# Optimization experiments

Hardware: AMD Instinct MI355X
Metric: run time of the kernel (lower is better)

Reference implementation:

```python
import jax, jax.numpy as jnp
import numpy as np

N_NODES = 50000
N_EDGES = 800000
FEAT = 128
HID = 128
N_GRAPHS = 512
N_CLASSES = 10
N_BLOCKS = 3
N_INNER = 2
BN_EPS = 1e-5


def setup_inputs() -> dict:
    key = jax.random.key(0)
    ks = jax.random.split(key, 16)
    return {
        "x": jax.random.normal(ks[0], (N_NODES, FEAT), dtype=jnp.float32),
        "edge_attr": jax.random.uniform(ks[1], (N_EDGES,), dtype=jnp.float32),
        "conv_w": jax.random.normal(ks[2], (N_BLOCKS, N_INNER, HID, HID), dtype=jnp.float32) * 0.05,
        "conv_b": jax.random.normal(ks[3], (N_BLOCKS, N_INNER, HID), dtype=jnp.float32) * 0.05,
        "jk_w": jax.random.normal(ks[4], (N_BLOCKS, N_INNER * HID, HID), dtype=jnp.float32) * 0.05,
        "jk_b": jax.random.normal(ks[5], (N_BLOCKS, HID), dtype=jnp.float32) * 0.05,
        "bn_gamma": jnp.ones((N_BLOCKS * HID,), dtype=jnp.float32),
        "bn_beta": jnp.zeros((N_BLOCKS * HID,), dtype=jnp.float32),
        "bn_mean": jnp.zeros((N_BLOCKS * HID,), dtype=jnp.float32),
        "bn_var": jnp.ones((N_BLOCKS * HID,), dtype=jnp.float32),
        "lin1_w": jax.random.normal(ks[6], (N_BLOCKS * HID, HID), dtype=jnp.float32) * 0.05,
        "lin1_b": jnp.zeros((HID,), dtype=jnp.float32),
        "lin2_w": jax.random.normal(ks[7], (HID, N_CLASSES), dtype=jnp.float32) * 0.05,
        "lin2_b": jnp.zeros((N_CLASSES,), dtype=jnp.float32),
        "edge_index": jax.random.randint(ks[8], (2, N_EDGES), 0, N_NODES, dtype=jnp.int32),
        "batch": jnp.sort(jax.random.randint(ks[9], (N_NODES,), 0, N_GRAPHS, dtype=jnp.int32)),
    }


def _gcn_conv(x, w, b, src, dst, ew):
    """GCNConv with edge weights and self-loops: D^-1/2 (A+I) D^-1/2 X W + b."""
    n = x.shape[0]
    xw = x @ w  # [N, H]
    deg = jax.ops.segment_sum(ew, dst, num_segments=n) + 1.0  # self-loop weight 1
    dinv = jax.lax.rsqrt(deg)  # [N]
    norm = dinv[src] * ew * dinv[dst]  # [E]
    agg = jax.ops.segment_sum(xw[src] * norm[:, None], dst, num_segments=n)
    agg = agg + xw * (dinv * dinv)[:, None]  # self-loop term
    return agg + b


def reference(x, edge_attr, conv_w, conv_b, jk_w, jk_b, bn_gamma, bn_beta,
              bn_mean, bn_var, lin1_w, lin1_b, lin2_w, lin2_b,
              edge_index, batch):
    src, dst = edge_index[0], edge_index[1]
    h = x
    pooled = []
    for l in range(N_BLOCKS):
        xs = []
        for k in range(N_INNER):
            h = jax.nn.relu(_gcn_conv(h, conv_w[l, k], conv_b[l, k], src, dst, edge_attr))
            xs.append(h)
        # JumpingKnowledge 'cat' + Linear + ReLU
        h = jax.nn.relu(jnp.concatenate(xs, axis=-1) @ jk_w[l] + jk_b[l])
        # global add pool per graph
        pooled.append(jax.ops.segment_sum(h, batch, num_segments=N_GRAPHS))
    z = jnp.concatenate(pooled, axis=1)  # [B, 3*HID]
    # BatchNorm1d (eval mode)
    z = (z - bn_mean) * jax.lax.rsqrt(bn_var + BN_EPS) * bn_gamma + bn_beta
    z = jax.nn.relu(z @ lin1_w + lin1_b)
    z = z @ lin2_w + lin2_b
    return jax.nn.softmax(z, axis=-1)
```

## Files before the change

kernel.cpp:

```cpp
#include <hip/hip_runtime.h>
#include <hip/hip_fp16.h>

static constexpr int NN = 50000;
static constexpr int NE = 800000;
static constexpr int NG = 512;

typedef unsigned int uint;
typedef unsigned short ushort;
typedef unsigned long long u64;
typedef __attribute__((ext_vector_type(8))) short short8;
typedef __attribute__((ext_vector_type(4))) float f32x4;

__device__ inline uint bfbits(float f) {
    uint u = __float_as_uint(f);
    return (u + 0x7fffu + ((u >> 16) & 1u)) >> 16;
}
__device__ inline float bflo(uint g) { return __uint_as_float(g << 16); }
__device__ inline float bfhi(uint g) { return __uint_as_float(g & 0xffff0000u); }
__device__ inline float bf2f(ushort s) { return __uint_as_float(((uint)s) << 16); }

__global__ void hist_kernel(const int* __restrict__ dst, const float* __restrict__ ew,
                            u64* __restrict__ pk, ushort* __restrict__ rankb, int nE)
{
    int i = blockIdx.x * blockDim.x + threadIdx.x;
    if (i < nE) {
        int d = dst[i];
        u64 v = (1ULL << 40) + (u64)(ew[i] * 16777216.0f + 0.5f);
        u64 old = atomicAdd(&pk[d], v);
        rankb[i] = (ushort)(old >> 40);
    }
}

__global__ __launch_bounds__(256) void scan_bsum_kernel(const u64* __restrict__ pk,
                                                        int* __restrict__ bsum,
                                                        float* __restrict__ dinv, int n)
{
    __shared__ int wred[4];
    int i = blockIdx.x * 256 + threadIdx.x;
    int v = 0;
    if (i < n) {
        u64 p = pk[i];
        v = (int)(p >> 40);
        float deg = (float)(p & 0xFFFFFFFFFFULL) * (1.0f / 16777216.0f) + 1.0f;
        dinv[i] = rsqrtf(deg);
    }
    int s = v;
    #pragma unroll
    for (int o = 32; o > 0; o >>= 1) s += __shfl_down(s, o, 64);
    int wid = threadIdx.x >> 6;
    if ((threadIdx.x & 63) == 0) wred[wid] = s;
    __syncthreads();
    if (threadIdx.x == 0)
        bsum[blockIdx.x] = wred[0] + wred[1] + wred[2] + wred[3];
}

__global__ __launch_bounds__(256) void scan_boff_kernel(const int* __restrict__ bsum,
                                                        int* __restrict__ boff, int nbs)
{
    __shared__ int sh[256];
    int tid = threadIdx.x;
    int v = (tid < nbs) ? bsum[tid] : 0;
    sh[tid] = v;
    __syncthreads();
    #pragma unroll
    for (int o = 1; o < 256; o <<= 1) {
        int t = (tid >= o) ? sh[tid - o] : 0;
        __syncthreads();
        sh[tid] += t;
        __syncthreads();
    }
    if (tid < nbs) boff[tid] = sh[tid] - v;
    if (tid == 255) boff[nbs] = sh[255];
}

__global__ __launch_bounds__(256) void scan_final_kernel(const u64* __restrict__ pk,
                                                         const int* __restrict__ boff,
                                                         int* __restrict__ rowptr,
                                                         int n, int nbs)
{
    __shared__ int sh[256];
    int tid = threadIdx.x;
    int i = blockIdx.x * 256 + tid;
    int v = (i < n) ? (int)(pk[i] >> 40) : 0;
    sh[tid] = v;
    __syncthreads();
    #pragma unroll
    for (int o = 1; o < 256; o <<= 1) {
        int t = (tid >= o) ? sh[tid - o] : 0;
        __syncthreads();
        sh[tid] += t;
        __syncthreads();
    }
    if (i < n) rowptr[i] = boff[blockIdx.x] + sh[tid] - v;
    if (blockIdx.x == 0 && tid == 0) rowptr[n] = boff[nbs];
}

__global__ void fill_kernel(const int* __restrict__ src, const int* __restrict__ dst,
                            const float* __restrict__ ew, const float* __restrict__ dinv,
                            const int* __restrict__ rowptr,
                            const ushort* __restrict__ rankb,
                            uint* __restrict__ ecv, int nE)
{
    int i = blockIdx.x * blockDim.x + threadIdx.x;
    if (i < nE) {
        int s = src[i], d = dst[i];
        int pos = rowptr[d] + (int)rankb[i];
        float v = ew[i] * dinv[s];
        ecv[pos] = (uint)s | ((uint)__half_as_ushort(__float2half_rn(v)) << 16);
    }
}

__global__ void cvtx_kernel(const float* __restrict__ x, ushort* __restrict__ xb, int n)
{
    int i = (blockIdx.x * blockDim.x + threadIdx.x) * 4;
    if (i < n) {
        float4 v = *(const float4*)&x[i];
        uint2 p;
        p.x = bfbits(v.x) | (bfbits(v.y) << 16);
        p.y = bfbits(v.z) | (bfbits(v.w) << 16);
        *(uint2*)&xb[i] = p;
    }
}

__global__ void wfrag_kernel(const float* __restrict__ src, ushort* __restrict__ dst,
                             int K, int wstride_src, int wstride_dst)
{
    int wid = blockIdx.y;
    const float* s = src + (size_t)wid * wstride_src;
    ushort* d = dst + (size_t)wid * wstride_dst;
    int i = blockIdx.x * 256 + threadIdx.x;
    int e = i & 7;
    int lane = (i >> 3) & 63;
    int rest = i >> 9;
    int nt = K >> 5;
    int t = rest % nt;
    int j = rest / nt;
    int k = t * 32 + (lane >> 4) * 8 + e;
    int col = j * 16 + (lane & 15);
    d[i] = (ushort)bfbits(s[(size_t)k * 128 + col]);
}

template<bool RELU, bool BIAS>
__global__ __launch_bounds__(256) void gemm_mfma_kernel(
    const ushort* __restrict__ Ab, int K, int lda,
    const ushort* __restrict__ Wb, const float* __restrict__ bias,
    ushort* __restrict__ outb, int nrows)
{
    const int wid  = threadIdx.x >> 6;
    const int lane = threadIdx.x & 63;
    const int row0 = blockIdx.x * 64 + wid * 16;
    const int c    = lane & 15;
    const int kg   = lane >> 4;
    int arow = row0 + c;
    if (arow >= nrows) arow = nrows - 1;
    const ushort* Aptr = Ab + (size_t)arow * lda + kg * 8;
    const int nt = K >> 5;

    f32x4 acc[8];
    #pragma unroll
    for (int j = 0; j < 8; ++j) acc[j] = (f32x4)0.f;

    for (int t = 0; t < nt; ++t) {
        short8 a = *(const short8*)(Aptr + t * 32);
        const ushort* Wp = Wb + ((size_t)t * 64 + lane) * 8;
        #pragma unroll
        for (int j = 0; j < 8; ++j) {
            short8 b = *(const short8*)(Wp + (size_t)j * nt * 512);
            acc[j] = __builtin_amdgcn_mfma_f32_16x16x32_bf16(a, b, acc[j], 0, 0, 0);
        }
    }
    #pragma unroll
    for (int r = 0; r < 4; ++r) {
        int orow = row0 + kg * 4 + r;
        if (orow >= nrows) continue;
        #pragma unroll
        for (int j = 0; j < 8; ++j) {
            float v = acc[j][r];
            int col = j * 16 + c;
            if (BIAS) v += bias[col];
            if (RELU) v = fmaxf(v, 0.f);
            outb[(size_t)orow * 128 + col] = (ushort)bfbits(v);
        }
    }
}

__global__ __launch_bounds__(256) void agg_kernel(
    const uint* __restrict__ xwb, const int* __restrict__ rowptr,
    const uint* __restrict__ ecv,
    const float* __restrict__ dinv, const float* __restrict__ bias,
    uint* __restrict__ outu, int ldo, int coff, int n)
{
    int node = (int)((blockIdx.x * (size_t)blockDim.x + threadIdx.x) >> 6);
    int lane = threadIdx.x & 63;
    if (node >= n) return;
    float d = dinv[node];
    uint  g = xwb[(size_t)node * 64 + lane];
    float bx = 0.f, by = 0.f;
    int e0 = rowptr[node], e1 = rowptr[node + 1];
    int e = e0;
    for (; e + 8 <= e1; e += 8) {
        uint rec[8];
        #pragma unroll
        for (int q = 0; q < 8; ++q) rec[q] = ecv[e + q];
        uint gq[8];
        #pragma unroll
        for (int q = 0; q < 8; ++q)
            gq[q] = xwb[(size_t)(rec[q] & 0xffffu) * 64 + lane];
        #pragma unroll
        for (int q = 0; q < 8; ++q) {
            float v = __half2float(__ushort_as_half((ushort)(rec[q] >> 16)));
            bx = fmaf(v, bflo(gq[q]), bx);
            by = fmaf(v, bfhi(gq[q]), by);
        }
    }
    for (; e + 4 <= e1; e += 4) {
        uint rec[4];
        #pragma unroll
        for (int q = 0; q < 4; ++q) rec[q] = ecv[e + q];
        uint gq[4];
        #pragma unroll
        for (int q = 0; q < 4; ++q)
            gq[q] = xwb[(size_t)(rec[q] & 0xffffu) * 64 + lane];
        #pragma unroll
        for (int q = 0; q < 4; ++q) {
            float v = __half2float(__ushort_as_half((ushort)(rec[q] >> 16)));
            bx = fmaf(v, bflo(gq[q]), bx);
            by = fmaf(v, bfhi(gq[q]), by);
        }
    }
    for (; e < e1; ++e) {
        uint rec = ecv[e];
        uint gg = xwb[(size_t)(rec & 0xffffu) * 64 + lane];
        float v = __half2float(__ushort_as_half((ushort)(rec >> 16)));
        bx = fmaf(v, bflo(gg), bx);
        by = fmaf(v, bfhi(gg), by);
    }
    float sw = d * d;
    float ax = fmaf(d, bx, bflo(g) * sw);
    float ay = fmaf(d, by, bfhi(g) * sw);
    float2 b = *(const float2*)&bias[lane * 2];
    ax = fmaxf(ax + b.x, 0.f);
    ay = fmaxf(ay + b.y, 0.f);
    outu[(size_t)node * ldo + coff + lane] = bfbits(ax) | (bfbits(ay) << 16);
}

static constexpr int NPP = 32;
__global__ __launch_bounds__(128) void pool_kernel(
    const ushort* __restrict__ h, const int* __restrict__ batch,
    float* __restrict__ z, int zoff, int n)
{
    int f  = threadIdx.x;
    int n0 = blockIdx.x * NPP;
    if (n0 >= n) return;
    int nend = n0 + NPP; if (nend > n) nend = n;
    int cur = batch[n0];
    float acc = 0.f;
    for (int node = n0; node < nend; ++node) {
        int b = batch[node];
        if (b != cur) {
            atomicAdd(&z[(size_t)cur * 384 + zoff + f], acc);
            acc = 0.f; cur = b;
        }
        acc += bf2f(h[(size_t)node * 128 + f]);
    }
    atomicAdd(&z[(size_t)cur * 384 + zoff + f], acc);
}

__global__ __launch_bounds__(128) void head_kernel(
    const float* __restrict__ z,
    const float* __restrict__ g,  const float* __restrict__ be,
    const float* __restrict__ mu, const float* __restrict__ var,
    const float* __restrict__ w1, const float* __restrict__ b1,
    const float* __restrict__ w2, const float* __restrict__ b2,
    float* __restrict__ out)
{
    int gi = blockIdx.x;
    int t  = threadIdx.x;
    __shared__ float zs[384];
    __shared__ float h1[128];
    __shared__ float lg[10];
    for (int i = t; i < 384; i += 128) {
        float v = z[(size_t)gi * 384 + i];
        v = (v - mu[i]) * rsqrtf(var[i] + 1e-5f) * g[i] + be[i];
        zs[i] = v;
    }
    __syncthreads();
    float acc = b1[t];
    for (int k = 0; k < 384; ++k) acc = fmaf(zs[k], w1[(size_t)k * 128 + t], acc);
    h1[t] = fmaxf(acc, 0.f);
    __syncthreads();
    if (t < 10) {
        float a2 = b2[t];
        for (int k = 0; k < 128; ++k) a2 = fmaf(h1[k], w2[(size_t)k * 10 + t], a2);
        lg[t] = a2;
    }
    __syncthreads();
    if (t == 0) {
        float m = lg[0];
        for (int i = 1; i < 10; ++i) m = fmaxf(m, lg[i]);
        float e[10], s = 0.f;
        for (int i = 0; i < 10; ++i) { e[i] = expf(lg[i] - m); s += e[i]; }
        float inv = 1.f / s;
        for (int i = 0; i < 10; ++i) out[(size_t)gi * 10 + i] = e[i] * inv;
    }
}

extern "C" void kernel_launch(void* const* d_in, const int* in_sizes, int n_in,
                              void* d_out, int out_size, void* d_ws, size_t ws_size,
                              hipStream_t stream)
{
    const float* x      = (const float*)d_in[0];
    const float* ea     = (const float*)d_in[1];
    const float* conv_w = (const float*)d_in[2];
    const float* conv_b = (const float*)d_in[3];
    const float* jk_w   = (const float*)d_in[4];
    const float* jk_b   = (const float*)d_in[5];
    const float* bn_g   = (const float*)d_in[6];
    const float* bn_b   = (const float*)d_in[7];
    const float* bn_m   = (const float*)d_in[8];
    const float* bn_v   = (const float*)d_in[9];
    const float* w1     = (const float*)d_in[10];
    const float* b1     = (const float*)d_in[11];
    const float* w2     = (const float*)d_in[12];
    const float* b2     = (const float*)d_in[13];
    const int*   eidx   = (const int*)d_in[14];
    const int*   batch  = (const int*)d_in[15];
    const int* srcv = eidx;
    const int* dstv = eidx + NE;
    float* out = (float*)d_out;

    char* ws = (char*)d_ws;
    size_t off = 0;
    auto alloc = [&](size_t b) { size_t o = off; off += (b + 511) & ~(size_t)511; return o; };
    u64*   pk     = (u64*)  (ws + alloc((size_t)NN * 8));
    float* z      = (float*)(ws + alloc((size_t)NG * 384 * 4));
    size_t zero_bytes = off;
    float* dinv   = (float*)(ws + alloc((size_t)NN * 4));
    int*   rowptr = (int*)  (ws + alloc((size_t)(NN + 1) * 4));
    ushort* rankb = (ushort*)(ws + alloc((size_t)NE * 2));
    uint*  ecv    = (uint*) (ws + alloc((size_t)NE * 4));
    ushort* xb    = (ushort*)(ws + alloc((size_t)NN * 128 * 2));
    ushort* wbc   = (ushort*)(ws + alloc((size_t)6 * 128 * 128 * 2));
    ushort* wbj   = (ushort*)(ws + alloc((size_t)3 * 256 * 128 * 2));
    uint*  xwb    = (uint*) (ws + alloc((size_t)NN * 64 * 4));
    uint*  xsb    = (uint*) (ws + alloc((size_t)NN * 128 * 4));
    ushort* houtb = (ushort*)(ws + alloc((size_t)NN * 128 * 2));
    int*   bsum   = (int*)  (ws + alloc((size_t)256 * 4));
    int*   boff   = (int*)  (ws + alloc((size_t)257 * 4));
    (void)ws_size; (void)in_sizes; (void)n_in; (void)out_size;

    hipMemsetAsync(d_ws, 0, zero_bytes, stream);

    const int EB  = (NE + 255) / 256;
    const int NB  = (NN + 255) / 256;
    hist_kernel<<<EB, 256, 0, stream>>>(dstv, ea, pk, rankb, NE);
    scan_bsum_kernel<<<NB, 256, 0, stream>>>(pk, bsum, dinv, NN);
    scan_boff_kernel<<<1, 256, 0, stream>>>(bsum, boff, NB);
    scan_final_kernel<<<NB, 256, 0, stream>>>(pk, boff, rowptr, NN, NB);
    fill_kernel<<<EB, 256, 0, stream>>>(srcv, dstv, ea, dinv, rowptr, rankb,
                                        ecv, NE);
    cvtx_kernel<<<(NN * 32 + 255) / 256, 256, 0, stream>>>(x, xb, NN * 128);
    wfrag_kernel<<<dim3(64, 6),  256, 0, stream>>>(conv_w, wbc, 128, 128 * 128, 128 * 128);
    wfrag_kernel<<<dim3(128, 3), 256, 0, stream>>>(jk_w,   wbj, 256, 256 * 128, 256 * 128);

    const int GB = (NN + 63) / 64;
    const int AB = (NN * 64 + 255) / 256;
    const int PB = (NN + NPP - 1) / NPP;

    const ushort* hin = xb;
    int lda = 128;
    for (int l = 0; l < 3; ++l) {
        for (int k = 0; k < 2; ++k) {
            gemm_mfma_kernel<false, false><<<GB, 256, 0, stream>>>(
                hin, 128, lda, wbc + (size_t)(l * 2 + k) * 128 * 128, nullptr,
                (ushort*)xwb, NN);
            agg_kernel<<<AB, 256, 0, stream>>>(
                xwb, rowptr, ecv, dinv, conv_b + (size_t)(l * 2 + k) * 128,
                xsb, 128, k * 64, NN);
            hin = (const ushort*)xsb;
            lda = 256;
        }
        gemm_mfma_kernel<true, true><<<GB, 256, 0, stream>>>(
            (const ushort*)xsb, 256, 256, wbj + (size_t)l * 256 * 128,
            jk_b + (size_t)l * 128, houtb, NN);
        pool_kernel<<<PB, 128, 0, stream>>>(houtb, batch, z, l * 128, NN);
        hin = houtb;
        lda = 128;
    }
    head_kernel<<<NG, 128, 0, stream>>>(z, bn_g, bn_b, bn_m, bn_v,
                                        w1, b1, w2, b2, out);
}
```

Baseline: 588.6 us.

## Fuse JK GEMM with pooling and next conv GEMM; merge prep kernels

```diff
diff --git a/kernel.cpp b/kernel.cpp
--- a/kernel.cpp
+++ b/kernel.cpp
@@ -19,116 +19,43 @@
 __device__ inline float bfhi(uint g) { return __uint_as_float(g & 0xffff0000u); }
 __device__ inline float bf2f(ushort s) { return __uint_as_float(((uint)s) << 16); }
 
-__global__ void hist_kernel(const int* __restrict__ dst, const float* __restrict__ ew,
-                            u64* __restrict__ pk, ushort* __restrict__ rankb, int nE)
-{
-    int i = blockIdx.x * blockDim.x + threadIdx.x;
-    if (i < nE) {
-        int d = dst[i];
-        u64 v = (1ULL << 40) + (u64)(ew[i] * 16777216.0f + 0.5f);
-        u64 old = atomicAdd(&pk[d], v);
-        rankb[i] = (ushort)(old >> 40);
-    }
-}
-
-__global__ __launch_bounds__(256) void scan_bsum_kernel(const u64* __restrict__ pk,
-                                                        int* __restrict__ bsum,
-                                                        float* __restrict__ dinv, int n)
-{
-    __shared__ int wred[4];
-    int i = blockIdx.x * 256 + threadIdx.x;
-    int v = 0;
-    if (i < n) {
-        u64 p = pk[i];
-        v = (int)(p >> 40);
-        float deg = (float)(p & 0xFFFFFFFFFFULL) * (1.0f / 16777216.0f) + 1.0f;
-        dinv[i] = rsqrtf(deg);
-    }
-    int s = v;
-    #pragma unroll
-    for (int o = 32; o > 0; o >>= 1) s += __shfl_down(s, o, 64);
-    int wid = threadIdx.x >> 6;
-    if ((threadIdx.x & 63) == 0) wred[wid] = s;
-    __syncthreads();
-    if (threadIdx.x == 0)
-        bsum[blockIdx.x] = wred[0] + wred[1] + wred[2] + wred[3];
-}
-
-__global__ __launch_bounds__(256) void scan_boff_kernel(const int* __restrict__ bsum,
-                                                        int* __restrict__ boff, int nbs)
-{
-    __shared__ int sh[256];
+static constexpr int EB  = (NE + 255) / 256;
+static constexpr int WBC = 6 * 64;
+static constexpr int WBJ = 3 * 128;
+
+__global__ __launch_bounds__(256) void prep_kernel(
+    const int* __restrict__ dst, const float* __restrict__ ew,
+    u64* __restrict__ pk, ushort* __restrict__ rankb,
+    const float* __restrict__ conv_w, ushort* __restrict__ wbc,
+    const float* __restrict__ jk_w, ushort* __restrict__ wbj)
+{
+    int b = blockIdx.x;
     int tid = threadIdx.x;
-    int v = (tid < nbs) ? bsum[tid] : 0;
-    sh[tid] = v;
-    __syncthreads();
-    #pragma unroll
-    for (int o = 1; o < 256; o <<= 1) {
-        int t = (tid >= o) ? sh[tid - o] : 0;
-        __syncthreads();
-        sh[tid] += t;
-        __syncthreads();
-    }
-    if (tid < nbs) boff[tid] = sh[tid] - v;
-    if (tid == 255) boff[nbs] = sh[255];
-}
-
-__global__ __launch_bounds__(256) void scan_final_kernel(const u64* __restrict__ pk,
-                                                         const int* __restrict__ boff,
-                                                         int* __restrict__ rowptr,
-                                                         int n, int nbs)
-{
-    __shared__ int sh[256];
-    int tid = threadIdx.x;
-    int i = blockIdx.x * 256 + tid;
-    int v = (i < n) ? (int)(pk[i] >> 40) : 0;
-    sh[tid] = v;
-    __syncthreads();
-    #pragma unroll
-    for (int o = 1; o < 256; o <<= 1) {
-        int t = (tid >= o) ? sh[tid - o] : 0;
-        __syncthreads();
-        sh[tid] += t;
-        __syncthreads();
-    }
-    if (i < n) rowptr[i] = boff[blockIdx.x] + sh[tid] - v;
-    if (blockIdx.x == 0 && tid == 0) rowptr[n] = boff[nbs];
-}
-
-__global__ void fill_kernel(const int* __restrict__ src, const int* __restrict__ dst,
-                            const float* __restrict__ ew, const float* __restrict__ dinv,
-                            const int* __restrict__ rowptr,
-                            const ushort* __restrict__ rankb,
-                            uint* __restrict__ ecv, int nE)
-{
-    int i = blockIdx.x * blockDim.x + threadIdx.x;
-    if (i < nE) {
-        int s = src[i], d = dst[i];
-        int pos = rowptr[d] + (int)rankb[i];
-        float v = ew[i] * dinv[s];
-        ecv[pos] = (uint)s | ((uint)__half_as_ushort(__float2half_rn(v)) << 16);
-    }
-}
-
-__global__ void cvtx_kernel(const float* __restrict__ x, ushort* __restrict__ xb, int n)
-{
-    int i = (blockIdx.x * blockDim.x + threadIdx.x) * 4;
-    if (i < n) {
-        float4 v = *(const float4*)&x[i];
-        uint2 p;
-        p.x = bfbits(v.x) | (bfbits(v.y) << 16);
-        p.y = bfbits(v.z) | (bfbits(v.w) << 16);
-        *(uint2*)&xb[i] = p;
-    }
-}
-
-__global__ void wfrag_kernel(const float* __restrict__ src, ushort* __restrict__ dst,
-                             int K, int wstride_src, int wstride_dst)
-{
-    int wid = blockIdx.y;
-    const float* s = src + (size_t)wid * wstride_src;
-    ushort* d = dst + (size_t)wid * wstride_dst;
-    int i = blockIdx.x * 256 + threadIdx.x;
+    if (b < EB) {
+        int i = b * 256 + tid;
+        if (i < NE) {
+            int d = dst[i];
+            u64 v = (1ULL << 40) + (u64)(ew[i] * 16777216.0f + 0.5f);
+            u64 old = atomicAdd(&pk[d], v);
+            rankb[i] = (ushort)(old >> 40);
+        }
+        return;
+    }
+    const float* s; ushort* d; int K, blk;
+    if (b < EB + WBC) {
+        int bb = b - EB;
+        int wid = bb >> 6; blk = bb & 63;
+        K = 128;
+        s = conv_w + (size_t)wid * 128 * 128;
+        d = wbc    + (size_t)wid * 128 * 128;
+    } else {
+        int bb = b - EB - WBC;
+        int wid = bb >> 7; blk = bb & 127;
+        K = 256;
+        s = jk_w + (size_t)wid * 256 * 128;
+        d = wbj  + (size_t)wid * 256 * 128;
+    }
+    int i = blk * 256 + tid;
     int e = i & 7;
     int lane = (i >> 3) & 63;
     int rest = i >> 9;
@@ -140,10 +67,92 @@
     d[i] = (ushort)bfbits(s[(size_t)k * 128 + col]);
 }
 
-template<bool RELU, bool BIAS>
-__global__ __launch_bounds__(256) void gemm_mfma_kernel(
-    const ushort* __restrict__ Ab, int K, int lda,
-    const ushort* __restrict__ Wb, const float* __restrict__ bias,
+__global__ __launch_bounds__(256) void scan_ab_kernel(
+    const u64* __restrict__ pk, int* __restrict__ bsum, float* __restrict__ dinv,
+    int* __restrict__ boff, uint* __restrict__ ctr, int n, int nbs)
+{
+    __shared__ int wred[4];
+    __shared__ int lastf;
+    int tid = threadIdx.x;
+    int i = blockIdx.x * 256 + tid;
+    int v = 0;
+    if (i < n) {
+        u64 p = pk[i];
+        v = (int)(p >> 40);
+        float deg = (float)(p & 0xFFFFFFFFFFULL) * (1.0f / 16777216.0f) + 1.0f;
+        dinv[i] = rsqrtf(deg);
+    }
+    int s = v;
+    #pragma unroll
+    for (int o = 32; o > 0; o >>= 1) s += __shfl_down(s, o, 64);
+    int wid = tid >> 6;
+    if ((tid & 63) == 0) wred[wid] = s;
+    __syncthreads();
+    if (tid == 0) {
+        bsum[blockIdx.x] = wred[0] + wred[1] + wred[2] + wred[3];
+        __threadfence();
+        uint old = atomicAdd(ctr, 1u);
+        lastf = (old == (uint)(gridDim.x - 1));
+    }
+    __syncthreads();
+    if (!lastf) return;
+    __threadfence();
+    __shared__ int sh[256];
+    int bv = (tid < nbs) ? bsum[tid] : 0;
+    sh[tid] = bv;
+    __syncthreads();
+    #pragma unroll
+    for (int o = 1; o < 256; o <<= 1) {
+        int t2 = (tid >= o) ? sh[tid - o] : 0;
+        __syncthreads();
+        sh[tid] += t2;
+        __syncthreads();
+    }
+    if (tid < nbs) boff[tid] = sh[tid] - bv;
+    if (tid == 255) boff[nbs] = sh[255];
+}
+
+__global__ __launch_bounds__(256) void scan_final_kernel(const u64* __restrict__ pk,
+                                                         const int* __restrict__ boff,
+                                                         int* __restrict__ rowptr,
+                                                         int n, int nbs)
+{
+    __shared__ int sh[256];
+    int tid = threadIdx.x;
+    int i = blockIdx.x * 256 + tid;
+    int v = (i < n) ? (int)(pk[i] >> 40) : 0;
+    sh[tid] = v;
+    __syncthreads();
+    #pragma unroll
+    for (int o = 1; o < 256; o <<= 1) {
+        int t = (tid >= o) ? sh[tid - o] : 0;
+        __syncthreads();
+        sh[tid] += t;
+        __syncthreads();
+    }
+    if (i < n) rowptr[i] = boff[blockIdx.x] + sh[tid] - v;
+    if (blockIdx.x == 0 && tid == 0) rowptr[n] = boff[nbs];
+}
+
+__global__ void fill_kernel(const int* __restrict__ src, const int* __restrict__ dst,
+                            const float* __restrict__ ew, const float* __restrict__ dinv,
+                            const int* __restrict__ rowptr,
+                            const ushort* __restrict__ rankb,
+                            uint* __restrict__ ecv, int nE)
+{
+    int i = blockIdx.x * blockDim.x + threadIdx.x;
+    if (i < nE) {
+        int s = src[i], d = dst[i];
+        int pos = rowptr[d] + (int)rankb[i];
+        float v = ew[i] * dinv[s];
+        ecv[pos] = (uint)s | ((uint)__half_as_ushort(__float2half_rn(v)) << 16);
+    }
+}
+
+template<bool AF32>
+__global__ __launch_bounds__(256) void conv_gemm_kernel(
+    const void* __restrict__ Aab, int K, int lda,
+    const ushort* __restrict__ Wb,
     ushort* __restrict__ outb, int nrows)
 {
     const int wid  = threadIdx.x >> 6;
@@ -153,7 +162,6 @@
     const int kg   = lane >> 4;
     int arow = row0 + c;
     if (arow >= nrows) arow = nrows - 1;
-    const ushort* Aptr = Ab + (size_t)arow * lda + kg * 8;
     const int nt = K >> 5;
 
     f32x4 acc[8];
@@ -161,7 +169,18 @@
     for (int j = 0; j < 8; ++j) acc[j] = (f32x4)0.f;
 
     for (int t = 0; t < nt; ++t) {
-        short8 a = *(const short8*)(Aptr + t * 32);
+        short8 a;
+        if (AF32) {
+            const float* Ap = (const float*)Aab + (size_t)arow * lda + kg * 8 + t * 32;
+            float4 f0 = *(const float4*)Ap;
+            float4 f1 = *(const float4*)(Ap + 4);
+            a[0] = (short)bfbits(f0.x); a[1] = (short)bfbits(f0.y);
+            a[2] = (short)bfbits(f0.z); a[3] = (short)bfbits(f0.w);
+            a[4] = (short)bfbits(f1.x); a[5] = (short)bfbits(f1.y);
+            a[6] = (short)bfbits(f1.z); a[7] = (short)bfbits(f1.w);
+        } else {
+            a = *(const short8*)((const ushort*)Aab + (size_t)arow * lda + kg * 8 + t * 32);
+        }
         const ushort* Wp = Wb + ((size_t)t * 64 + lane) * 8;
         #pragma unroll
         for (int j = 0; j < 8; ++j) {
@@ -174,13 +193,102 @@
         int orow = row0 + kg * 4 + r;
         if (orow >= nrows) continue;
         #pragma unroll
+        for (int j = 0; j < 8; ++j)
+            outb[(size_t)orow * 128 + j * 16 + c] = (ushort)bfbits(acc[j][r]);
+    }
+}
+
+template<bool CHAIN>
+__global__ __launch_bounds__(256) void jk_fused_kernel(
+    const ushort* __restrict__ xsb, const ushort* __restrict__ wbj,
+    const float* __restrict__ jkb,
+    const int* __restrict__ batch, float* __restrict__ z, int zoff,
+    const ushort* __restrict__ wnext, ushort* __restrict__ xwb_out, int nrows)
+{
+    __shared__ __align__(16) ushort hl[64 * 128];
+    __shared__ int sb[64];
+    const int tid  = threadIdx.x;
+    const int wid  = tid >> 6;
+    const int lane = tid & 63;
+    const int rowb = blockIdx.x * 64;
+    const int row0 = rowb + wid * 16;
+    const int c    = lane & 15;
+    const int kg   = lane >> 4;
+
+    if (tid < 64) {
+        int rr = rowb + tid;
+        sb[tid] = (rr < nrows) ? batch[rr] : -1;
+    }
+    int arow = row0 + c;
+    if (arow >= nrows) arow = nrows - 1;
+    const ushort* Aptr = xsb + (size_t)arow * 256 + kg * 8;
+
+    f32x4 acc[8];
+    #pragma unroll
+    for (int j = 0; j < 8; ++j) acc[j] = (f32x4)0.f;
+    for (int t = 0; t < 8; ++t) {
+        short8 a = *(const short8*)(Aptr + t * 32);
+        const ushort* Wp = wbj + ((size_t)t * 64 + lane) * 8;
+        #pragma unroll
         for (int j = 0; j < 8; ++j) {
-            float v = acc[j][r];
-            int col = j * 16 + c;
-            if (BIAS) v += bias[col];
-            if (RELU) v = fmaxf(v, 0.f);
-            outb[(size_t)orow * 128 + col] = (ushort)bfbits(v);
-        }
+            short8 b = *(const short8*)(Wp + (size_t)j * 8 * 512);
+            acc[j] = __builtin_amdgcn_mfma_f32_16x16x32_bf16(a, b, acc[j], 0, 0, 0);
+        }
+    }
+    #pragma unroll
+    for (int r = 0; r < 4; ++r) {
+        int rl = wid * 16 + kg * 4 + r;
+        #pragma unroll
+        for (int j = 0; j < 8; ++j) {
+            float v = fmaxf(acc[j][r] + jkb[j * 16 + c], 0.f);
+            uint byte = ((uint)(rl * 256 + (j * 16 + c) * 2)) ^ ((uint)(rl & 7) << 4);
+            *(ushort*)((char*)hl + byte) = (ushort)bfbits(v);
+        }
+    }
+    __syncthreads();
+
+    if (CHAIN) {
+        f32x4 ac2[8];
+        #pragma unroll
+        for (int j = 0; j < 8; ++j) ac2[j] = (f32x4)0.f;
+        int rl2 = wid * 16 + c;
+        uint rx = (uint)(rl2 & 7) << 4;
+        #pragma unroll
+        for (int t = 0; t < 4; ++t) {
+            uint byte = ((uint)(rl2 * 256 + (kg * 8 + t * 32) * 2)) ^ rx;
+            short8 a = *(const short8*)((char*)hl + byte);
+            const ushort* Wp = wnext + ((size_t)t * 64 + lane) * 8;
+            #pragma unroll
+            for (int j = 0; j < 8; ++j) {
+                short8 b = *(const short8*)(Wp + (size_t)j * 4 * 512);
+                ac2[j] = __builtin_amdgcn_mfma_f32_16x16x32_bf16(a, b, ac2[j], 0, 0, 0);
+            }
+        }
+        #pragma unroll
+        for (int r = 0; r < 4; ++r) {
+            int orow = row0 + kg * 4 + r;
+            if (orow >= nrows) continue;
+            #pragma unroll
+            for (int j = 0; j < 8; ++j)
+                xwb_out[(size_t)orow * 128 + j * 16 + c] = (ushort)bfbits(ac2[j][r]);
+        }
+    }
+
+    if (tid < 128) {
+        int f = tid;
+        int nend = nrows - rowb; if (nend > 64) nend = 64;
+        int cur = sb[0];
+        float acc2 = 0.f;
+        for (int rl = 0; rl < nend; ++rl) {
+            int bb = sb[rl];
+            if (bb != cur) {
+                atomicAdd(&z[(size_t)cur * 384 + zoff + f], acc2);
+                acc2 = 0.f; cur = bb;
+            }
+            uint byte = ((uint)(rl * 256 + f * 2)) ^ ((uint)(rl & 7) << 4);
+            acc2 += bf2f(*(const ushort*)((const char*)hl + byte));
+        }
+        atomicAdd(&z[(size_t)cur * 384 + zoff + f], acc2);
     }
 }
 
@@ -188,7 +296,7 @@
     const uint* __restrict__ xwb, const int* __restrict__ rowptr,
     const uint* __restrict__ ecv,
     const float* __restrict__ dinv, const float* __restrict__ bias,
-    uint* __restrict__ outu, int ldo, int coff, int n)
+    uint* __restrict__ outu, int coff, int n)
 {
     int node = (int)((blockIdx.x * (size_t)blockDim.x + threadIdx.x) >> 6);
     int lane = threadIdx.x & 63;
@@ -198,16 +306,16 @@
     float bx = 0.f, by = 0.f;
     int e0 = rowptr[node], e1 = rowptr[node + 1];
     int e = e0;
-    for (; e + 8 <= e1; e += 8) {
-        uint rec[8];
-        #pragma unroll
-        for (int q = 0; q < 8; ++q) rec[q] = ecv[e + q];
-        uint gq[8];
-        #pragma unroll
-        for (int q = 0; q < 8; ++q)
+    for (; e + 16 <= e1; e += 16) {
+        uint rec[16];
+        #pragma unroll
+        for (int q = 0; q < 16; ++q) rec[q] = ecv[e + q];
+        uint gq[16];
+        #pragma unroll
+        for (int q = 0; q < 16; ++q)
             gq[q] = xwb[(size_t)(rec[q] & 0xffffu) * 64 + lane];
         #pragma unroll
-        for (int q = 0; q < 8; ++q) {
+        for (int q = 0; q < 16; ++q) {
             float v = __half2float(__ushort_as_half((ushort)(rec[q] >> 16)));
             bx = fmaf(v, bflo(gq[q]), bx);
             by = fmaf(v, bfhi(gq[q]), by);
@@ -241,29 +349,7 @@
     float2 b = *(const float2*)&bias[lane * 2];
     ax = fmaxf(ax + b.x, 0.f);
     ay = fmaxf(ay + b.y, 0.f);
-    outu[(size_t)node * ldo + coff + lane] = bfbits(ax) | (bfbits(ay) << 16);
-}
-
-static constexpr int NPP = 32;
-__global__ __launch_bounds__(128) void pool_kernel(
-    const ushort* __restrict__ h, const int* __restrict__ batch,
-    float* __restrict__ z, int zoff, int n)
-{
-    int f  = threadIdx.x;
-    int n0 = blockIdx.x * NPP;
-    if (n0 >= n) return;
-    int nend = n0 + NPP; if (nend > n) nend = n;
-    int cur = batch[n0];
-    float acc = 0.f;
-    for (int node = n0; node < nend; ++node) {
-        int b = batch[node];
-        if (b != cur) {
-            atomicAdd(&z[(size_t)cur * 384 + zoff + f], acc);
-            acc = 0.f; cur = b;
-        }
-        acc += bf2f(h[(size_t)node * 128 + f]);
-    }
-    atomicAdd(&z[(size_t)cur * 384 + zoff + f], acc);
+    outu[(size_t)node * 128 + coff + lane] = bfbits(ax) | (bfbits(ay) << 16);
 }
 
 __global__ __launch_bounds__(128) void head_kernel(
@@ -334,58 +420,56 @@
     auto alloc = [&](size_t b) { size_t o = off; off += (b + 511) & ~(size_t)511; return o; };
     u64*   pk     = (u64*)  (ws + alloc((size_t)NN * 8));
     float* z      = (float*)(ws + alloc((size_t)NG * 384 * 4));
+    uint*  ctr    = (uint*) (ws + alloc(512));
     size_t zero_bytes = off;
     float* dinv   = (float*)(ws + alloc((size_t)NN * 4));
     int*   rowptr = (int*)  (ws + alloc((size_t)(NN + 1) * 4));
     ushort* rankb = (ushort*)(ws + alloc((size_t)NE * 2));
     uint*  ecv    = (uint*) (ws + alloc((size_t)NE * 4));
-    ushort* xb    = (ushort*)(ws + alloc((size_t)NN * 128 * 2));
     ushort* wbc   = (ushort*)(ws + alloc((size_t)6 * 128 * 128 * 2));
     ushort* wbj   = (ushort*)(ws + alloc((size_t)3 * 256 * 128 * 2));
     uint*  xwb    = (uint*) (ws + alloc((size_t)NN * 64 * 4));
     uint*  xsb    = (uint*) (ws + alloc((size_t)NN * 128 * 4));
-    ushort* houtb = (ushort*)(ws + alloc((size_t)NN * 128 * 2));
     int*   bsum   = (int*)  (ws + alloc((size_t)256 * 4));
     int*   boff   = (int*)  (ws + alloc((size_t)257 * 4));
     (void)ws_size; (void)in_sizes; (void)n_in; (void)out_size;
 
     hipMemsetAsync(d_ws, 0, zero_bytes, stream);
 
-    const int EB  = (NE + 255) / 256;
-    const int NB  = (NN + 255) / 256;
-    hist_kernel<<<EB, 256, 0, stream>>>(dstv, ea, pk, rankb, NE);
-    scan_bsum_kernel<<<NB, 256, 0, stream>>>(pk, bsum, dinv, NN);
-    scan_boff_kernel<<<1, 256, 0, stream>>>(bsum, boff, NB);
+    const int NB = (NN + 255) / 256;
+    prep_kernel<<<EB + WBC + WBJ, 256, 0, stream>>>(dstv, ea, pk, rankb,
+                                                    conv_w, wbc, jk_w, wbj);
+    scan_ab_kernel<<<NB, 256, 0, stream>>>(pk, bsum, dinv, boff, ctr, NN, NB);
     scan_final_kernel<<<NB, 256, 0, stream>>>(pk, boff, rowptr, NN, NB);
     fill_kernel<<<EB, 256, 0, stream>>>(srcv, dstv, ea, dinv, rowptr, rankb,
                                         ecv, NE);
-    cvtx_kernel<<<(NN * 32 + 255) / 256, 256, 0, stream>>>(x, xb, NN * 128);
-    wfrag_kernel<<<dim3(64, 6),  256, 0, stream>>>(conv_w, wbc, 128, 128 * 128, 128 * 128);
-    wfrag_kernel<<<dim3(128, 3), 256, 0, stream>>>(jk_w,   wbj, 256, 256 * 128, 256 * 128);
 
     const int GB = (NN + 63) / 64;
     const int AB = (NN * 64 + 255) / 256;
-    const int PB = (NN + NPP - 1) / NPP;
-
-    const ushort* hin = xb;
-    int lda = 128;
+
+    conv_gemm_kernel<true><<<GB, 256, 0, stream>>>(x, 128, 128, wbc,
+                                                   (ushort*)xwb, NN);
     for (int l = 0; l < 3; ++l) {
-        for (int k = 0; k < 2; ++k) {
-            gemm_mfma_kernel<false, false><<<GB, 256, 0, stream>>>(
-                hin, 128, lda, wbc + (size_t)(l * 2 + k) * 128 * 128, nullptr,
-                (ushort*)xwb, NN);
-            agg_kernel<<<AB, 256, 0, stream>>>(
-                xwb, rowptr, ecv, dinv, conv_b + (size_t)(l * 2 + k) * 128,
-                xsb, 128, k * 64, NN);
-            hin = (const ushort*)xsb;
-            lda = 256;
-        }
-        gemm_mfma_kernel<true, true><<<GB, 256, 0, stream>>>(
-            (const ushort*)xsb, 256, 256, wbj + (size_t)l * 256 * 128,
-            jk_b + (size_t)l * 128, houtb, NN);
-        pool_kernel<<<PB, 128, 0, stream>>>(houtb, batch, z, l * 128, NN);
-        hin = houtb;
-        lda = 128;
+        agg_kernel<<<AB, 256, 0, stream>>>(
+            xwb, rowptr, ecv, dinv, conv_b + (size_t)(l * 2 + 0) * 128,
+            xsb, 0, NN);
+        conv_gemm_kernel<false><<<GB, 256, 0, stream>>>(
+            (const ushort*)xsb, 128, 256, wbc + (size_t)(l * 2 + 1) * 128 * 128,
+            (ushort*)xwb, NN);
+        agg_kernel<<<AB, 256, 0, stream>>>(
+            xwb, rowptr, ecv, dinv, conv_b + (size_t)(l * 2 + 1) * 128,
+            xsb, 64, NN);
+        if (l < 2) {
+            jk_fused_kernel<true><<<GB, 256, 0, stream>>>(
+                (const ushort*)xsb, wbj + (size_t)l * 256 * 128,
+                jk_b + (size_t)l * 128, batch, z, l * 128,
+                wbc + (size_t)(l + 1) * 2 * 128 * 128, (ushort*)xwb, NN);
+        } else {
+            jk_fused_kernel<false><<<GB, 256, 0, stream>>>(
+                (const ushort*)xsb, wbj + (size_t)l * 256 * 128,
+                jk_b + (size_t)l * 128, batch, z, l * 128,
+                nullptr, nullptr, NN);
+        }
     }
     head_kernel<<<NG, 128, 0, stream>>>(z, bn_g, bn_b, bn_m, bn_v,
                                         w1, b1, w2, b2, out);
```

Result: faster. 514.6 us (-12.6%).
